# Performance work log

Hardware: AMD Instinct MI355X
Metric: run time of the kernel (lower is better)

The kernel has to match this reference:

```python
import jax, jax.numpy as jnp
import numpy as np

KS = 3          # kernel_size
PAD = 1         # padding
N = KS * KS     # 9 sampling points
S2 = 2 ** 0.5
ANGLES = [0, 45, 90, 135, 180]

# angle-dependent extra offsets (x, y), indexed by angle // 45
_OFF = {
    0: ([0.0] * 9, [0.0] * 9),
    1: ([1 - S2, 1 - S2 * 0.5, 1, -S2 * 0.5, 0, S2 * 0.5, -1, S2 * 0.5 - 1, S2 - 1],
        [1, S2 * 0.5, S2 - 1, 1 - S2 * 0.5, 0, S2 * 0.5 - 1, 1 - S2, -S2 * 0.5, -1]),
    2: ([0, 1, 2, -1, 0, 1, -2, -1, 0],
        [2, 1, 0, 1, 0, -1, 0, -1, -2]),
    3: ([1, 1 + S2 * 0.5, 1 + S2, -S2 * 0.5, 0, S2 * 0.5, -1 - S2, -1 - S2 * 0.5, -1],
        [1 + S2, S2 * 0.5, -1, 1 + S2 * 0.5, 0, -1 - S2 * 0.5, 1, -S2 * 0.5, 1 + S2]),
    4: ([2, 2, 2, 0, 0, 0, -2, -2, -2],
        [2, 0, -2, 2, 0, -2, 2, 0, -2]),
}


def _deform_sample(x, angle):
    """Bilinear gather of the rotated 3x3 sampling grid -> (b,c,h*KS,w*KS)."""
    b, c, h, w = x.shape
    xp = jnp.pad(x, ((0, 0), (0, 0), (PAD, PAD), (PAD, PAD)))  # zero padding
    ph, pw = h + 2 * PAD, w + 2 * PAD

    ox_l, oy_l = _OFF[angle // 45]
    ox = jnp.asarray(np.array(ox_l, dtype=np.float32))
    oy = jnp.asarray(np.array(oy_l, dtype=np.float32))

    rng = np.arange(-(KS - 1) // 2, (KS - 1) // 2 + 1)
    pnx_np, pny_np = np.meshgrid(rng, rng, indexing='ij')  # torch default 'ij'
    pnx = jnp.asarray(pnx_np.reshape(-1).astype(np.float32))
    pny = jnp.asarray(pny_np.reshape(-1).astype(np.float32))

    # p = p_0 + p_n + offset ; keep x as (h,1,N) and y as (1,w,N), broadcast later
    px = jnp.arange(1, h + 1, dtype=jnp.float32)[:, None, None] + (pnx + ox)[None, None, :]  # (h,1,N)
    py = jnp.arange(1, w + 1, dtype=jnp.float32)[None, :, None] + (pny + oy)[None, None, :]  # (1,w,N)

    fx, fy = jnp.floor(px), jnp.floor(py)
    ql_x = jnp.clip(fx, 0, ph - 1)       # left-top row
    qr_x = jnp.clip(fx + 1, 0, ph - 1)   # right-bottom row
    ql_y = jnp.clip(fy, 0, pw - 1)
    qr_y = jnp.clip(fy + 1, 0, pw - 1)

    pxc = jnp.clip(px, 0, ph - 1)
    pyc = jnp.clip(py, 0, pw - 1)

    g_lt = (1 + (ql_x - pxc)) * (1 + (ql_y - pyc))  # (h,w,N) after broadcast
    g_rb = (1 - (qr_x - pxc)) * (1 - (qr_y - pyc))
    g_lb = (1 + (ql_x - pxc)) * (1 - (qr_y - pyc))
    g_rt = (1 - (qr_x - pxc)) * (1 + (ql_y - pyc))

    xf = xp.reshape(b, c, ph * pw)

    def gather(qx, qy):
        idx = qx.astype(jnp.int32) * pw + qy.astype(jnp.int32)      # (h,w,N)
        idx = jnp.broadcast_to(idx, (h, w, N)).reshape(-1)
        return jnp.take(xf, idx, axis=2).reshape(b, c, h, w, N)

    xo = (jnp.broadcast_to(g_lt, (h, w, N))[None, None] * gather(ql_x, ql_y)
          + jnp.broadcast_to(g_rb, (h, w, N))[None, None] * gather(qr_x, qr_y)
          + jnp.broadcast_to(g_lb, (h, w, N))[None, None] * gather(ql_x, qr_y)
          + jnp.broadcast_to(g_rt, (h, w, N))[None, None] * gather(qr_x, ql_y))

    # (b,c,h,w,N) -> (b,c,h*KS,w*KS) matching torch _reshape_x_offset
    xo = xo.reshape(b, c, h, w, KS, KS).transpose(0, 1, 2, 4, 3, 5).reshape(b, c, h * KS, w * KS)
    return xo


def _conv(xo, weight):
    # baseline_conv: stride=1, padding=0, no bias
    return jax.lax.conv_general_dilated(
        xo, weight, window_strides=(1, 1), padding='VALID',
        dimension_numbers=('NCHW', 'OIHW', 'NCHW'))


def setup_inputs() -> dict:
    key = jax.random.key(0)
    kx, kw = jax.random.split(key)
    x = jax.random.normal(kx, (2, 256, 64, 64), dtype=jnp.float32)
    weight = jax.random.normal(kw, (256, 256, 3, 3), dtype=jnp.float32) * 0.02
    return {"x": x, "weight": weight}


def reference(x, weight):
    return tuple(_conv(_deform_sample(x, a), weight) for a in ANGLES)
```

## Files before the change

### kernel.cpp

```cpp
#include <hip/hip_runtime.h>
#include <hip/hip_bf16.h>
#include <stdint.h>


#define S2F 1.41421356237309515f

__constant__ float c_ox[5][9] = {
  {0.f,0.f,0.f,0.f,0.f,0.f,0.f,0.f,0.f},
  {1.f-S2F, 1.f-S2F*0.5f, 1.f, -S2F*0.5f, 0.f, S2F*0.5f, -1.f, S2F*0.5f-1.f, S2F-1.f},
  {0.f,1.f,2.f,-1.f,0.f,1.f,-2.f,-1.f,0.f},
  {1.f, 1.f+S2F*0.5f, 1.f+S2F, -S2F*0.5f, 0.f, S2F*0.5f, -1.f-S2F, -1.f-S2F*0.5f, -1.f},
  {2.f,2.f,2.f,0.f,0.f,0.f,-2.f,-2.f,-2.f}
};
__constant__ float c_oy[5][9] = {
  {0.f,0.f,0.f,0.f,0.f,0.f,0.f,0.f,0.f},
  {1.f, S2F*0.5f, S2F-1.f, 1.f-S2F*0.5f, 0.f, S2F*0.5f-1.f, 1.f-S2F, -S2F*0.5f, -1.f},
  {2.f,1.f,0.f,1.f,0.f,-1.f,0.f,-1.f,-2.f},
  {1.f+S2F, S2F*0.5f, -1.f, 1.f+S2F*0.5f, 0.f, -1.f-S2F*0.5f, 1.f, -S2F*0.5f, 1.f+S2F},
  {2.f,0.f,-2.f,2.f,0.f,-2.f,2.f,0.f,-2.f}
};

typedef __bf16 bf16x8_t __attribute__((ext_vector_type(8)));
typedef float f32x4_t __attribute__((ext_vector_type(4)));

typedef const __attribute__((address_space(1))) void* as1cp;
typedef __attribute__((address_space(3))) void* as3p;

__device__ __forceinline__ void gload16(const void* g, void* l) {
  __builtin_amdgcn_global_load_lds((as1cp)g, (as3p)l, 16, 0, 0);
}

__global__ void k_transpose(const float* __restrict__ x, float* __restrict__ xT) {
  const int v = blockIdx.x, u = blockIdx.y, b = blockIdx.z;
  const int ic = threadIdx.x;
  xT[(((b*64 + u)*64 + v)*256) + ic] =
      x[(((b*256 + ic)*64 + u)*64) + v];
}

__global__ void k_wconv(const float* __restrict__ w, __hip_bfloat16* __restrict__ wb) {
  const int tid = blockIdx.x*256 + threadIdx.x;
  const int t = tid >> 16;
  const int rem = tid & 65535;
  const int oc = rem >> 8;
  const int ic = rem & 255;
  wb[tid] = __float2bfloat16(w[(oc*256 + ic)*9 + t]);
}

__global__ void k_sample(const float* __restrict__ xT,
                         __hip_bfloat16* __restrict__ xo, int a0)
{
  const int aidx = a0 + blockIdx.z;
  __hip_bfloat16* xoa = xo + (size_t)blockIdx.z * (2ull*192*192*256);

  const int tid = threadIdx.x;
  const int ic = (tid & 63) * 4;
  const int j = blockIdx.x*4 + (tid >> 6);
  const int i = blockIdx.y;

  const int a = i / 3, r = i - 3*a;
  const int bc = j / 3, s = j - 3*bc;
  const int n = r*3 + s;
  const float px = (float)(a + r) + c_ox[aidx][n];
  const float py = (float)(bc + s) + c_oy[aidx][n];
  const float fx = floorf(px), fy = floorf(py);
  const float pxc = fminf(fmaxf(px, 0.f), 65.f);
  const float pyc = fminf(fmaxf(py, 0.f), 65.f);
  const int qlx = (int)fminf(fmaxf(fx,      0.f), 65.f);
  const int qrx = (int)fminf(fmaxf(fx + 1.f, 0.f), 65.f);
  const int qly = (int)fminf(fmaxf(fy,      0.f), 65.f);
  const int qry = (int)fminf(fmaxf(fy + 1.f, 0.f), 65.f);
  const float wlx = 1.f + (float)qlx - pxc;
  const float wrx = 1.f - (float)qrx + pxc;
  const float wly = 1.f + (float)qly - pyc;
  const float wry = 1.f - (float)qry + pyc;
  const float glt = wlx*wly, grb = wrx*wry, glb = wlx*wry, grt = wrx*wly;

  const bool inxl = (qlx >= 1) && (qlx <= 64);
  const bool inxr = (qrx >= 1) && (qrx <= 64);
  const bool inyl = (qly >= 1) && (qly <= 64);
  const bool inyr = (qry >= 1) && (qry <= 64);

  const f32x4_t zero = (f32x4_t){0.f,0.f,0.f,0.f};
  #pragma unroll
  for (int b = 0; b < 2; ++b) {
    const float* xb = xT + (size_t)b * (64*64*256);
    f32x4_t vlt = (inxl && inyl) ? *(const f32x4_t*)&xb[((qlx-1)*64 + (qly-1))*256 + ic] : zero;
    f32x4_t vrb = (inxr && inyr) ? *(const f32x4_t*)&xb[((qrx-1)*64 + (qry-1))*256 + ic] : zero;
    f32x4_t vlb = (inxl && inyr) ? *(const f32x4_t*)&xb[((qlx-1)*64 + (qry-1))*256 + ic] : zero;
    f32x4_t vrt = (inxr && inyl) ? *(const f32x4_t*)&xb[((qrx-1)*64 + (qly-1))*256 + ic] : zero;
    ushort4 pk;
    float v0 = glt*vlt[0] + grb*vrb[0] + glb*vlb[0] + grt*vrt[0];
    float v1 = glt*vlt[1] + grb*vrb[1] + glb*vlb[1] + grt*vrt[1];
    float v2 = glt*vlt[2] + grb*vrb[2] + glb*vlb[2] + grt*vrt[2];
    float v3 = glt*vlt[3] + grb*vrb[3] + glb*vlb[3] + grt*vrt[3];
    pk.x = __hip_bfloat16_raw(__float2bfloat16(v0)).x;
    pk.y = __hip_bfloat16_raw(__float2bfloat16(v1)).x;
    pk.z = __hip_bfloat16_raw(__float2bfloat16(v2)).x;
    pk.w = __hip_bfloat16_raw(__float2bfloat16(v3)).x;
    *(ushort4*)&xoa[(((size_t)b*192 + i)*192 + j)*256 + ic] = pk;
  }
}

__global__ __launch_bounds__(256, 2) void k_conv(
    const __hip_bfloat16* __restrict__ xo,
    const __hip_bfloat16* __restrict__ wb,
    float* __restrict__ out)
{
  __shared__ __align__(16) char smem[66048];
  const int tid = threadIdx.x;
  const int nt = blockIdx.x & 1;
  const int ct = blockIdx.x >> 1;
  const int i0 = blockIdx.y * 2;
  const int z  = blockIdx.z;
  const int oc0 = nt * 128;
  const int j0 = ct * 64;

  const int q8   = tid >> 3;
  const int slot = tid & 7;
  const int wv   = tid >> 6;
  const int sw   = slot ^ (q8 & 7);

  const char* xob = (const char*)xo + (size_t)z * 18874368u;
  const char* wbc = (const char*)wb;

  int arow[4], acol[4], brow[4];
  #pragma unroll
  for (int p = 0; p < 4; ++p) {
    const int m = p*32 + q8;
    arow[p] = i0 + (m >> 6);
    acol[p] = j0 + (m & 63);
    brow[p] = oc0 + m;
  }

  f32x4_t acc[4][4];
  #pragma unroll
  for (int fm = 0; fm < 4; ++fm)
    #pragma unroll
    for (int fn = 0; fn < 4; ++fn)
      acc[fm][fn] = (f32x4_t){0.f, 0.f, 0.f, 0.f};

  const int lane = tid & 63;
  const int lrow = lane & 15;
  const int lk   = lane >> 4;
  const int wm   = wv >> 1;
  const int wn   = wv & 1;

  auto stage = [&](int kk, int cur) {
    const int icg = kk / 9;
    const int t   = kk - icg*9;
    const int ki = t / 3, kj = t - 3*ki;
    char* sa = smem + cur*16384 + wv*1024;
    char* sb = smem + 32768 + cur*16384 + wv*1024;
    #pragma unroll
    for (int p = 0; p < 4; ++p) {
      int col = acol[p] + kj; col = (col > 191) ? 191 : col;
      const char* ga = xob + (((arow[p] + ki)*192 + col)*256 + icg*64)*2 + sw*16;
      gload16(ga, sa + p*4096);
      const char* gb = wbc + ((t*256 + brow[p])*256 + icg*64)*2 + sw*16;
      gload16(gb, sb + p*4096);
    }
  };

  auto compute = [&](int cur) {
    const char* sa = smem + cur*16384;
    const char* sb = smem + 32768 + cur*16384;
    bf16x8_t af[4][2], bfr[4][2];
    #pragma unroll
    for (int f = 0; f < 4; ++f) {
      const int m = wm*64 + f*16 + lrow;
      const int n = wn*64 + f*16 + lrow;
      #pragma unroll
      for (int ks = 0; ks < 2; ++ks) {
        af[f][ks]  = *(const bf16x8_t*)(sa + m*128 + (((ks*4 + lk) ^ (m & 7)) * 16));
        bfr[f][ks] = *(const bf16x8_t*)(sb + n*128 + (((ks*4 + lk) ^ (n & 7)) * 16));
      }
    }
    #pragma unroll
    for (int fm = 0; fm < 4; ++fm)
      #pragma unroll
      for (int fn = 0; fn < 4; ++fn)
        #pragma unroll
        for (int ks = 0; ks < 2; ++ks)
          acc[fm][fn] = __builtin_amdgcn_mfma_f32_16x16x32_bf16(
              af[fm][ks], bfr[fn][ks], acc[fm][fn], 0, 0, 0);
  };

  stage(0, 0);
  __syncthreads();
  for (int kk = 0; kk < 36; ++kk) {
    const int cur = kk & 1;
    if (kk < 35) stage(kk + 1, cur ^ 1);
    compute(cur);
    __syncthreads();
  }

  float* eps = (float*)smem;
  #pragma unroll
  for (int fm = 0; fm < 4; ++fm)
    #pragma unroll
    for (int fn = 0; fn < 4; ++fn)
      #pragma unroll
      for (int r = 0; r < 4; ++r)
        eps[(wn*64 + fn*16 + lrow)*129 + (wm*64 + fm*16 + lk*4 + r)] = acc[fm][fn][r];
  __syncthreads();

  float* outb = out + (size_t)z * 9241600u;
  #pragma unroll
  for (int pass = 0; pass < 16; ++pass) {
    const int ocw = pass*8 + (tid >> 5);
    const int m4  = (tid & 31) * 4;
    const int di  = m4 >> 6, jc = m4 & 63;
    const int i = i0 + di, j = j0 + jc;
    const float v0 = eps[ocw*129 + m4 + 0];
    const float v1 = eps[ocw*129 + m4 + 1];
    const float v2 = eps[ocw*129 + m4 + 2];
    const float v3 = eps[ocw*129 + m4 + 3];
    float* dst = outb + ((size_t)(oc0 + ocw)*190 + i)*190 + j;
    if (j + 3 < 190) {
      *(float2*)dst       = make_float2(v0, v1);
      *(float2*)(dst + 2) = make_float2(v2, v3);
    } else {
      if (j     < 190) dst[0] = v0;
      if (j + 1 < 190) dst[1] = v1;
      if (j + 2 < 190) dst[2] = v2;
      if (j + 3 < 190) dst[3] = v3;
    }
  }
}

extern "C" void kernel_launch(void* const* d_in, const int* in_sizes, int n_in,
                              void* d_out, int out_size, void* d_ws, size_t ws_size,
                              hipStream_t stream)
{
  const float* x = (const float*)d_in[0];
  const float* w = (const float*)d_in[1];
  float* out = (float*)d_out;

  char* ws = (char*)d_ws;
  float*          xT = (float*)ws;
  __hip_bfloat16* wb = (__hip_bfloat16*)(ws + 8388608);
  __hip_bfloat16* xo = (__hip_bfloat16*)(ws + 9568256);

  const bool merged = (ws_size >= 198311936ull);

  k_transpose<<<dim3(64, 64, 2), 256, 0, stream>>>(x, xT);
  k_wconv<<<2304, 256, 0, stream>>>(w, wb);

  if (merged) {
    k_sample<<<dim3(48, 192, 5), 256, 0, stream>>>(xT, xo, 0);
    k_conv<<<dim3(6, 95, 10), 256, 0, stream>>>(xo, wb, out);
  } else {
    for (int aidx = 0; aidx < 5; ++aidx) {
      k_sample<<<dim3(48, 192, 1), 256, 0, stream>>>(xT, xo, aidx);
      k_conv<<<dim3(6, 95, 2), 256, 0, stream>>>(xo, wb, out + (size_t)aidx * 18483200u);
    }
  }
}
```

Before: 543.0 us.

## Enlarge conv tile to 256x128 using 32x32x16 MFMA with 32-wide K steps

The implicit-GEMM conv kernel now covers four output rows per block instead of two (a 256-pixel M tile) and steps K by 32 channels over 72 iterations instead of 64 over 36. It switches from 16x16x32 to 32x32x16 bf16 MFMA with larger per-wave fragments, and the LDS footprint shrinks. The epilogue writes accumulators through LDS one wave-quadrant at a time with contiguous row stores. The aim is more reuse of weight and activation loads per MFMA and fewer blocks. The cost is more barrier syncs per block and a serialized four-pass epilogue.

```diff
diff --git a/kernel.cpp b/kernel.cpp
--- a/kernel.cpp
+++ b/kernel.cpp
@@ -22,6 +22,7 @@
 
 typedef __bf16 bf16x8_t __attribute__((ext_vector_type(8)));
 typedef float f32x4_t __attribute__((ext_vector_type(4)));
+typedef float f32x16_t __attribute__((ext_vector_type(16)));
 
 typedef const __attribute__((address_space(1))) void* as1cp;
 typedef __attribute__((address_space(3))) void* as3p;
@@ -101,129 +102,117 @@
   }
 }
 
-__global__ __launch_bounds__(256, 2) void k_conv(
+__global__ __launch_bounds__(256, 2) void k_conv8(
     const __hip_bfloat16* __restrict__ xo,
     const __hip_bfloat16* __restrict__ wb,
     float* __restrict__ out)
 {
-  __shared__ __align__(16) char smem[66048];
+  __shared__ __align__(16) char smem[49152];
   const int tid = threadIdx.x;
   const int nt = blockIdx.x & 1;
   const int ct = blockIdx.x >> 1;
-  const int i0 = blockIdx.y * 2;
+  const int i0 = blockIdx.y * 4;
   const int z  = blockIdx.z;
   const int oc0 = nt * 128;
   const int j0 = ct * 64;
 
-  const int q8   = tid >> 3;
-  const int slot = tid & 7;
-  const int wv   = tid >> 6;
-  const int sw   = slot ^ (q8 & 7);
+  const int w = tid >> 6, l = tid & 63;
+  const int l31 = l & 31, hi = l >> 5;
+  const int wm = w >> 1, wn = w & 1;
 
   const char* xob = (const char*)xo + (size_t)z * 18874368u;
   const char* wbc = (const char*)wb;
 
-  int arow[4], acol[4], brow[4];
-  #pragma unroll
-  for (int p = 0; p < 4; ++p) {
-    const int m = p*32 + q8;
-    arow[p] = i0 + (m >> 6);
-    acol[p] = j0 + (m & 63);
-    brow[p] = oc0 + m;
-  }
-
-  f32x4_t acc[4][4];
-  #pragma unroll
-  for (int fm = 0; fm < 4; ++fm)
-    #pragma unroll
-    for (int fn = 0; fn < 4; ++fn)
-      acc[fm][fn] = (f32x4_t){0.f, 0.f, 0.f, 0.f};
-
-  const int lane = tid & 63;
-  const int lrow = lane & 15;
-  const int lk   = lane >> 4;
-  const int wm   = wv >> 1;
-  const int wn   = wv & 1;
+  const int aCol = j0 + (tid >> 2);
+  const int sOff = ((tid & 3) ^ ((tid >> 2) & 3)) * 16;
+  const int bOc0 = (oc0 + (tid >> 2)) * 512;
+  char* const dA = smem + w*1024;
+  char* const dB = smem + 32768 + w*1024;
 
   auto stage = [&](int kk, int cur) {
     const int icg = kk / 9;
     const int t   = kk - icg*9;
-    const int ki = t / 3, kj = t - 3*ki;
-    char* sa = smem + cur*16384 + wv*1024;
-    char* sb = smem + 32768 + cur*16384 + wv*1024;
+    const int ki = (t >= 6) ? 2 : ((t >= 3) ? 1 : 0);
+    const int kj = t - ki*3;
+    const int icoff = icg*64 + sOff;
+    char* Ad = dA + cur*16384;
+    char* Bd = dB + cur*8192;
+    int j = aCol + kj; if (j > 191) j = 191;
     #pragma unroll
     for (int p = 0; p < 4; ++p) {
-      int col = acol[p] + kj; col = (col > 191) ? 191 : col;
-      const char* ga = xob + (((arow[p] + ki)*192 + col)*256 + icg*64)*2 + sw*16;
-      gload16(ga, sa + p*4096);
-      const char* gb = wbc + ((t*256 + brow[p])*256 + icg*64)*2 + sw*16;
-      gload16(gb, sb + p*4096);
-    }
+      int i = i0 + p + ki; if (i > 191) i = 191;
+      gload16(xob + (size_t)(((i*192 + j) << 9) + icoff), Ad + p*4096);
+    }
+    const char* bs = wbc + t*131072 + icoff;
+    gload16(bs + bOc0,         Bd);
+    gload16(bs + bOc0 + 32768, Bd + 4096);
   };
 
+  f32x16_t acc[4][2];
+  #pragma unroll
+  for (int mf = 0; mf < 4; ++mf)
+    #pragma unroll
+    for (int nf = 0; nf < 2; ++nf)
+      #pragma unroll
+      for (int v = 0; v < 16; ++v)
+        acc[mf][nf][v] = 0.f;
+
+  const int rofA = (wm*128 + l31) * 64;
+  const int rofB = (wn*64  + l31) * 64;
+
   auto compute = [&](int cur) {
-    const char* sa = smem + cur*16384;
-    const char* sb = smem + 32768 + cur*16384;
-    bf16x8_t af[4][2], bfr[4][2];
+    const char* Ab = smem + cur*16384;
+    const char* Bb = smem + 32768 + cur*8192;
     #pragma unroll
-    for (int f = 0; f < 4; ++f) {
-      const int m = wm*64 + f*16 + lrow;
-      const int n = wn*64 + f*16 + lrow;
+    for (int ks = 0; ks < 2; ++ks) {
+      const int sl = (((ks*2 + hi) ^ (l31 & 3)) * 16);
+      const bf16x8_t b0 = *(const bf16x8_t*)(Bb + rofB + sl);
+      const bf16x8_t b1 = *(const bf16x8_t*)(Bb + rofB + 2048 + sl);
       #pragma unroll
-      for (int ks = 0; ks < 2; ++ks) {
-        af[f][ks]  = *(const bf16x8_t*)(sa + m*128 + (((ks*4 + lk) ^ (m & 7)) * 16));
-        bfr[f][ks] = *(const bf16x8_t*)(sb + n*128 + (((ks*4 + lk) ^ (n & 7)) * 16));
+      for (int mf = 0; mf < 4; ++mf) {
+        const bf16x8_t a = *(const bf16x8_t*)(Ab + rofA + mf*2048 + sl);
+        acc[mf][0] = __builtin_amdgcn_mfma_f32_32x32x16_bf16(a, b0, acc[mf][0], 0, 0, 0);
+        acc[mf][1] = __builtin_amdgcn_mfma_f32_32x32x16_bf16(a, b1, acc[mf][1], 0, 0, 0);
       }
     }
-    #pragma unroll
-    for (int fm = 0; fm < 4; ++fm)
-      #pragma unroll
-      for (int fn = 0; fn < 4; ++fn)
-        #pragma unroll
-        for (int ks = 0; ks < 2; ++ks)
-          acc[fm][fn] = __builtin_amdgcn_mfma_f32_16x16x32_bf16(
-              af[fm][ks], bfr[fn][ks], acc[fm][fn], 0, 0, 0);
   };
 
   stage(0, 0);
   __syncthreads();
-  for (int kk = 0; kk < 36; ++kk) {
+  for (int kk = 0; kk < 72; ++kk) {
     const int cur = kk & 1;
-    if (kk < 35) stage(kk + 1, cur ^ 1);
+    if (kk < 71) stage(kk + 1, cur ^ 1);
     compute(cur);
     __syncthreads();
   }
 
   float* eps = (float*)smem;
+  float* outb = out + (size_t)z * 9241600u;
+  const int ocr = tid >> 2, q = tid & 3;
+
   #pragma unroll
-  for (int fm = 0; fm < 4; ++fm)
-    #pragma unroll
-    for (int fn = 0; fn < 4; ++fn)
+  for (int pass = 0; pass < 4; ++pass) {
+    const int hm = pass >> 1, hn = pass & 1;
+    __syncthreads();
+    if (wm == hm && wn == hn) {
       #pragma unroll
-      for (int r = 0; r < 4; ++r)
-        eps[(wn*64 + fn*16 + lrow)*129 + (wm*64 + fm*16 + lk*4 + r)] = acc[fm][fn][r];
-  __syncthreads();
-
-  float* outb = out + (size_t)z * 9241600u;
-  #pragma unroll
-  for (int pass = 0; pass < 16; ++pass) {
-    const int ocw = pass*8 + (tid >> 5);
-    const int m4  = (tid & 31) * 4;
-    const int di  = m4 >> 6, jc = m4 & 63;
-    const int i = i0 + di, j = j0 + jc;
-    const float v0 = eps[ocw*129 + m4 + 0];
-    const float v1 = eps[ocw*129 + m4 + 1];
-    const float v2 = eps[ocw*129 + m4 + 2];
-    const float v3 = eps[ocw*129 + m4 + 3];
-    float* dst = outb + ((size_t)(oc0 + ocw)*190 + i)*190 + j;
-    if (j + 3 < 190) {
-      *(float2*)dst       = make_float2(v0, v1);
-      *(float2*)(dst + 2) = make_float2(v2, v3);
-    } else {
-      if (j     < 190) dst[0] = v0;
-      if (j + 1 < 190) dst[1] = v1;
-      if (j + 2 < 190) dst[2] = v2;
-      if (j + 3 < 190) dst[3] = v3;
+      for (int mf = 0; mf < 4; ++mf)
+        #pragma unroll
+        for (int nf = 0; nf < 2; ++nf)
+          #pragma unroll
+          for (int qv = 0; qv < 4; ++qv)
+            *(f32x4_t*)&eps[(nf*32 + l31)*132 + mf*32 + qv*8 + 4*hi] =
+                (f32x4_t){acc[mf][nf][qv*4+0], acc[mf][nf][qv*4+1],
+                          acc[mf][nf][qv*4+2], acc[mf][nf][qv*4+3]};
+    }
+    __syncthreads();
+    const int i = i0 + hm*2 + (q >> 1);
+    if (i < 190) {
+      float* dst = outb + (size_t)(oc0 + hn*64 + ocr)*36100u + i*190 + j0 + (q&1)*32;
+      const float* src = eps + ocr*132 + q*32;
+      const int kmax = (ct == 2 && (q & 1)) ? 30 : 32;
+      for (int k = 0; k < kmax; k += 2)
+        *(float2*)(dst + k) = make_float2(src[k], src[k + 1]);
     }
   }
 }
@@ -248,11 +237,11 @@
 
   if (merged) {
     k_sample<<<dim3(48, 192, 5), 256, 0, stream>>>(xT, xo, 0);
-    k_conv<<<dim3(6, 95, 10), 256, 0, stream>>>(xo, wb, out);
+    k_conv8<<<dim3(6, 48, 10), 256, 0, stream>>>(xo, wb, out);
   } else {
     for (int aidx = 0; aidx < 5; ++aidx) {
       k_sample<<<dim3(48, 192, 1), 256, 0, stream>>>(xT, xo, aidx);
-      k_conv<<<dim3(6, 95, 2), 256, 0, stream>>>(xo, wb, out + (size_t)aidx * 18483200u);
-    }
-  }
-}
+      k_conv8<<<dim3(6, 48, 2), 256, 0, stream>>>(xo, wb, out + (size_t)aidx * 18483200u);
+    }
+  }
+}
```

Measured after the change: 910.4 us. 1.68x slower.
